# Performance work log

Measured on AMD Instinct MI355X. Metric: run time of the kernel, lower is better.

The kernel has to match this reference:

```python
import jax, jax.numpy as jnp
import numpy as np

DIM = 768
HEADS = 12
TOPK = 32


def setup_inputs() -> dict:
    key = jax.random.key(0)
    k1, k2, k3 = jax.random.split(key, 3)
    B, hw, T = 8, 576, 4
    N = hw + T * hw
    x = jax.random.normal(k1, (B, N, DIM), dtype=jnp.float32)
    qkv_w = jax.random.normal(k2, (3 * DIM, DIM), dtype=jnp.float32) * 0.02
    proj_w = jax.random.normal(k3, (DIM, DIM), dtype=jnp.float32) * 0.02
    proj_b = jnp.zeros((DIM,), dtype=jnp.float32)
    return {"x": x, "qkv_w": qkv_w, "proj_w": proj_w, "proj_b": proj_b, "T": T, "hw": hw}


def _query_topk_every_frame(attn, hw, T):
    # attn: [B, H, hw, hw + T*hw]
    B, H, n1, _ = attn.shape
    qa = attn[..., :hw]                       # [B,H,hw,hw] query self part
    ma = attn[..., hw:].reshape(B, H, n1, T, hw)  # per-frame memory scores
    vals, idx = jax.lax.top_k(ma, TOPK)       # [B,H,hw,T,K]
    cat = jnp.concatenate([qa, vals.reshape(B, H, n1, T * TOPK)], axis=-1)
    sm = jax.nn.softmax(cat, axis=-1)         # softmax over hw + T*K survivors
    qa2 = sm[..., :hw]
    tv = sm[..., hw:].reshape(B, H, n1, T, TOPK)
    # scatter normalized top-k values back into dense per-frame affinity
    bi = jnp.arange(B)[:, None, None, None, None]
    hi = jnp.arange(H)[None, :, None, None, None]
    ni = jnp.arange(n1)[None, None, :, None, None]
    ti = jnp.arange(T)[None, None, None, :, None]
    aff = jnp.zeros_like(ma).at[bi, hi, ni, ti, idx].set(tv)
    return jnp.concatenate([qa2, aff.reshape(B, H, n1, T * hw)], axis=-1)


def reference(x, qkv_w, proj_w, proj_b, T, hw):
    B, N, C = x.shape
    assert N == hw + T * hw
    hd = C // HEADS
    scale = hd ** -0.5
    qkv = (x @ qkv_w.T).reshape(B, N, 3, HEADS, hd).transpose(2, 0, 3, 1, 4)
    q, k, v = qkv[0], qkv[1], qkv[2]          # each [B,H,N,hd]
    query_q = q[:, :, :hw]                    # [B,H,hw,hd]
    attn = jnp.einsum('bhqd,bhkd->bhqk', query_q, k) * scale  # [B,H,hw,N]
    attn = _query_topk_every_frame(attn, hw, T)
    out = jnp.einsum('bhqk,bhkd->bhqd', attn, v)  # [B,H,hw,hd]
    query = out.transpose(0, 2, 1, 3).reshape(B, hw, C)
    query = query @ proj_w.T + proj_b
    # memory tokens pass through unchanged
    return jnp.concatenate([query, x[:, hw:]], axis=1)
```

## Files before the change

kernel.cpp:

```cpp
#include <hip/hip_runtime.h>
#include <hip/hip_bf16.h>


using s16x8 = __attribute__((ext_vector_type(8))) short;
using f32x4 = __attribute__((ext_vector_type(4))) float;
typedef unsigned short u16;

#define MFMA_B16(A,B,C) __builtin_amdgcn_mfma_f32_16x16x32_bf16(A,B,C,0,0,0)

__device__ __forceinline__ u16 f2bf(float f) {
  unsigned u = __float_as_uint(f);
  u += 0x7FFFu + ((u >> 16) & 1u);
  return (u16)(u >> 16);
}
__device__ __forceinline__ float bf2f(u16 h) {
  return __uint_as_float(((unsigned)h) << 16);
}
__device__ __forceinline__ int lanes_below(unsigned long long m) {
  return __builtin_amdgcn_mbcnt_hi((unsigned)(m >> 32),
         __builtin_amdgcn_mbcnt_lo((unsigned)m, 0));
}

__global__ __launch_bounds__(256) void cvt_kernel(const float* __restrict__ src,
                                                  u16* __restrict__ dst, int n4) {
  int i = blockIdx.x * blockDim.x + threadIdx.x;
  if (i >= n4) return;
  float4 v = ((const float4*)src)[i];
  unsigned lo = (unsigned)f2bf(v.x) | ((unsigned)f2bf(v.y) << 16);
  unsigned hi = (unsigned)f2bf(v.z) | ((unsigned)f2bf(v.w) << 16);
  uint2 o; o.x = lo; o.y = hi;
  ((uint2*)dst)[i] = o;
}

__global__ __launch_bounds__(256) void copy_tail_kernel(const float* __restrict__ x,
                                                        float* __restrict__ out) {
  int i = blockIdx.x * blockDim.x + threadIdx.x;
  int b = i / 442368;
  int off = i - b * 442368;
  size_t e = (size_t)b * 552960 + 110592 + off;
  ((float4*)out)[e] = ((const float4*)x)[e];
}

template<int MODE>
__global__ __launch_bounds__(256) void gemm_nt(
    const u16* __restrict__ A, const u16* __restrict__ Bw,
    const float* __restrict__ bias,
    u16* __restrict__ qbuf, u16* __restrict__ kbuf,
    u16* __restrict__ vbuf, u16* __restrict__ vtb,
    float* __restrict__ fout)
{
  constexpr int LDT = 72;
  __shared__ __align__(16) u16 sA[64 * LDT];
  __shared__ __align__(16) u16 sB[64 * LDT];
  const int n0 = blockIdx.x * 64;
  const int m0 = blockIdx.y * 64;
  if (MODE == 0) {
    if (n0 < 768 && (blockIdx.y % 45) >= 9) return;
  }
  const int tid = threadIdx.x;
  const int w = tid >> 6, lane = tid & 63;
  const int srow = tid >> 2, scb = tid & 3;
  const int mh = (w >> 1) * 32, nh = (w & 1) * 32;
  f32x4 z = {0.f, 0.f, 0.f, 0.f};
  f32x4 acc[2][2] = {{z, z}, {z, z}};

  for (int k0 = 0; k0 < 768; k0 += 64) {
    __syncthreads();
    #pragma unroll
    for (int c = scb; c < 8; c += 4) {
      *(int4*)&sA[srow * LDT + c * 8] =
          *(const int4*)&A[(size_t)(m0 + srow) * 768 + k0 + c * 8];
      *(int4*)&sB[srow * LDT + c * 8] =
          *(const int4*)&Bw[(size_t)(n0 + srow) * 768 + k0 + c * 8];
    }
    __syncthreads();
    #pragma unroll
    for (int kk = 0; kk < 2; ++kk) {
      const int ko = kk * 32 + (lane >> 4) * 8;
      s16x8 a0 = *(const s16x8*)&sA[(mh +      (lane & 15)) * LDT + ko];
      s16x8 a1 = *(const s16x8*)&sA[(mh + 16 + (lane & 15)) * LDT + ko];
      s16x8 b0 = *(const s16x8*)&sB[(nh +      (lane & 15)) * LDT + ko];
      s16x8 b1 = *(const s16x8*)&sB[(nh + 16 + (lane & 15)) * LDT + ko];
      acc[0][0] = MFMA_B16(a0, b0, acc[0][0]);
      acc[0][1] = MFMA_B16(a0, b1, acc[0][1]);
      acc[1][0] = MFMA_B16(a1, b0, acc[1][0]);
      acc[1][1] = MFMA_B16(a1, b1, acc[1][1]);
    }
  }

  if (MODE == 0) {
    const int which = n0 / 768;
    const int h = (n0 % 768) >> 6;
    #pragma unroll
    for (int mi = 0; mi < 2; ++mi)
      #pragma unroll
      for (int ni = 0; ni < 2; ++ni)
        #pragma unroll
        for (int r = 0; r < 4; ++r) {
          const int gm = m0 + mh + mi * 16 + (lane >> 4) * 4 + r;
          const int d  = nh + ni * 16 + (lane & 15);
          const int b  = gm / 2880;
          const int rr = gm - b * 2880;
          const float c = acc[mi][ni][r];
          if (which == 0) {
            if (rr < 576)
              qbuf[((size_t)(b * 12 + h) * 576 + rr) * 64 + d] = f2bf(c * 0.125f);
          } else if (which == 1) {
            kbuf[((size_t)(b * 12 + h) * 2880 + rr) * 64 + d] = f2bf(c);
          } else {
            const u16 bv = f2bf(c);
            vbuf[((size_t)(b * 12 + h) * 2880 + rr) * 64 + d] = bv;
            if (rr < 576)
              vtb[((size_t)((b * 12 + h) * 64 + d)) * 576 + rr] = bv;
          }
        }
  } else {
    #pragma unroll
    for (int mi = 0; mi < 2; ++mi)
      #pragma unroll
      for (int ni = 0; ni < 2; ++ni)
        #pragma unroll
        for (int r = 0; r < 4; ++r) {
          const int gm = m0 + mh + mi * 16 + (lane >> 4) * 4 + r;
          const int gn = n0 + nh + ni * 16 + (lane & 15);
          const int b = gm / 576;
          const int q = gm - b * 576;
          fout[((size_t)b * 2880 + q) * 768 + gn] = acc[mi][ni][r] + bias[gn];
        }
  }
}

__global__ __launch_bounds__(256, 6) void attn_kernel(
    const u16* __restrict__ qbuf, const u16* __restrict__ kbuf,
    const u16* __restrict__ vbuf, const u16* __restrict__ vtb,
    u16* __restrict__ aout)
{
  constexpr int PST = 584;
  __shared__ __align__(16) u16 s_p[16 * PST];
  __shared__ float s_selp[16][32];
  __shared__ u16   s_seli[16][32];
  __shared__ float s_O[16][64];
  __shared__ float s_denom[16];

  const int bid = blockIdx.x;
  const int L = (bid & 7) * 432 + (bid >> 3);
  const int qt = L % 36;
  const int h  = (L / 36) % 12;
  const int b  = L / 432;
  const int bh = b * 12 + h;
  const int q0 = qt * 16;
  const int tid = threadIdx.x, w = tid >> 6, lane = tid & 63;
  const int l15 = lane & 15, rg = lane >> 4;
  const int ko = rg * 8;

  #pragma unroll
  for (int i = 0; i < 4; ++i) ((float*)s_O)[tid + 256 * i] = 0.f;

  const u16* qp = qbuf + ((size_t)bh * 576 + q0) * 64;
  s16x8 aQ[2];
  aQ[0] = *(const s16x8*)&qp[l15 * 64 + ko];
  aQ[1] = *(const s16x8*)&qp[l15 * 64 + 32 + ko];

  const u16* kp = kbuf + (size_t)bh * 2880 * 64;
  f32x4 zz = {0.f, 0.f, 0.f, 0.f};
  f32x4 accO = zz;

  for (int c = 0; c < 5; ++c) {
    #pragma unroll 3
    for (int t = 0; t < 9; ++t) {
      const int wk = w * 144 + t * 16;
      const u16* kr = kp + (size_t)(c * 576 + wk + l15) * 64 + ko;
      s16x8 kf0 = *(const s16x8*)&kr[0];
      s16x8 kf1 = *(const s16x8*)&kr[32];
      f32x4 a0 = zz;
      a0 = MFMA_B16(aQ[0], kf0, a0);
      a0 = MFMA_B16(aQ[1], kf1, a0);
      if (c == 0) {
        #pragma unroll
        for (int r = 0; r < 4; ++r)
          s_p[(rg * 4 + r) * PST + wk + l15] = f2bf(__expf(a0[r]));
      } else {
        #pragma unroll
        for (int r = 0; r < 4; ++r)
          s_p[(rg * 4 + r) * PST + wk + l15] = f2bf(a0[r]);
      }
    }
    __syncthreads();

    if (c == 0) {
      const u16* vt = vtb + ((size_t)bh * 64 + w * 16 + l15) * 576;
      #pragma unroll 3
      for (int k0 = 0; k0 < 576; k0 += 32) {
        s16x8 vf = *(const s16x8*)&vt[k0 + ko];
        s16x8 pa = *(const s16x8*)&s_p[l15 * PST + k0 + ko];
        accO = MFMA_B16(pa, vf, accO);
      }
      #pragma unroll
      for (int ri = 0; ri < 4; ++ri) {
        const int q = w * 4 + ri;
        float s = 0.f;
        #pragma unroll
        for (int j = 0; j < 9; ++j) s += bf2f(s_p[q * PST + lane + 64 * j]);
        #pragma unroll
        for (int off = 1; off < 64; off <<= 1) s += __shfl_xor(s, off);
        if (lane == 0) s_denom[q] = s;
      }
    } else {
      for (int ri = 0; ri < 4; ++ri) {
        const int q = w * 4 + ri;
        unsigned key[9];
        #pragma unroll
        for (int j = 0; j < 9; ++j) {
          unsigned raw = s_p[q * PST + lane + 64 * j];
          key[j] = (raw & 0x8000u) ? (raw ^ 0xFFFFu) : (raw | 0x8000u);
        }
        unsigned prefix = 0;
        for (int bit = 15; bit >= 0; --bit) {
          const unsigned cand = prefix | (1u << bit);
          int cnt = 0;
          #pragma unroll
          for (int j = 0; j < 9; ++j)
            cnt += __popcll(__ballot(key[j] >= cand));
          if (cnt >= 32) prefix = cand;
          if (cnt == 32) break;
        }
        unsigned long long gtm[9], eqm[9];
        int cnt_gt = 0;
        #pragma unroll
        for (int j = 0; j < 9; ++j) {
          gtm[j] = __ballot(key[j] > prefix);
          eqm[j] = __ballot(key[j] == prefix);
          cnt_gt += __popcll(gtm[j]);
        }
        int run_gt = 0, run_eq = cnt_gt;
        float dsum = 0.f;
        #pragma unroll
        for (int j = 0; j < 9; ++j) {
          int slot = -1;
          if (key[j] > prefix) slot = run_gt + lanes_below(gtm[j]);
          else if (key[j] == prefix) {
            const int s2 = run_eq + lanes_below(eqm[j]);
            if (s2 < 32) slot = s2;
          }
          if (slot >= 0) {
            const unsigned kk = key[j];
            const u16 raw = (kk & 0x8000u) ? (u16)(kk ^ 0x8000u) : (u16)(kk ^ 0xFFFFu);
            const float p = __expf(bf2f(raw));
            dsum += p;
            s_selp[q][slot] = p;
            s_seli[q][slot] = (u16)(c * 576 + lane + 64 * j);
          }
          run_gt += __popcll(gtm[j]);
          run_eq += __popcll(eqm[j]);
        }
        #pragma unroll
        for (int off = 1; off < 64; off <<= 1) dsum += __shfl_xor(dsum, off);
        if (lane == 0) s_denom[q] += dsum;
        float ga = 0.f;
        const u16* vp = vbuf + (size_t)bh * 2880 * 64 + lane;
        #pragma unroll 8
        for (int i = 0; i < 32; ++i) {
          const float p = s_selp[q][i];
          const int keyi = s_seli[q][i];
          ga += p * bf2f(vp[(size_t)keyi * 64]);
        }
        s_O[q][lane] += ga;
      }
    }
    __syncthreads();
  }

  const int d = w * 16 + l15;
  #pragma unroll
  for (int r = 0; r < 4; ++r) {
    const int row = rg * 4 + r;
    const float val = (accO[r] + s_O[row][d]) / s_denom[row];
    aout[((size_t)(b * 576 + q0 + row)) * 768 + h * 64 + d] = f2bf(val);
  }
}

extern "C" void kernel_launch(void* const* d_in, const int* in_sizes, int n_in,
                              void* d_out, int out_size, void* d_ws, size_t ws_size,
                              hipStream_t stream)
{
  const float* x      = (const float*)d_in[0];
  const float* qkv_w  = (const float*)d_in[1];
  const float* proj_w = (const float*)d_in[2];
  const float* proj_b = (const float*)d_in[3];
  float* out = (float*)d_out;

  char* ws = (char*)d_ws;
  size_t off = 0;
  auto alloc = [&](size_t bytes) -> void* {
    void* p = ws + off;
    off += (bytes + 255) & ~(size_t)255;
    return p;
  };
  u16* xb   = (u16*)alloc((size_t)23040 * 768 * 2);
  u16* wqb  = (u16*)alloc((size_t)2304 * 768 * 2);
  u16* wpb  = (u16*)alloc((size_t)768 * 768 * 2);
  u16* qbuf = (u16*)alloc((size_t)96 * 576 * 64 * 2);
  u16* vtb  = (u16*)alloc((size_t)96 * 64 * 576 * 2);
  u16* aout = (u16*)alloc((size_t)4608 * 768 * 2);
  u16* kbuf = (u16*)d_out;
  u16* vbuf = kbuf + (size_t)96 * 2880 * 64;

  cvt_kernel<<<17280, 256, 0, stream>>>(x, xb, 17694720 / 4);
  cvt_kernel<<<1728, 256, 0, stream>>>(qkv_w, wqb, 1769472 / 4);
  cvt_kernel<<<576, 256, 0, stream>>>(proj_w, wpb, 589824 / 4);
  gemm_nt<0><<<dim3(36, 360), 256, 0, stream>>>(xb, wqb, nullptr,
                                                qbuf, kbuf, vbuf, vtb, nullptr);
  attn_kernel<<<3456, 256, 0, stream>>>(qbuf, kbuf, vbuf, vtb, aout);
  gemm_nt<1><<<dim3(12, 72), 256, 0, stream>>>(aout, wpb, proj_b,
                                               nullptr, nullptr, nullptr, nullptr, out);
  copy_tail_kernel<<<13824, 256, 0, stream>>>(x, out);
}
```

Before: 552.8 us.

## Replace sparse top-k gather with dense masked P·V MFMA per memory frame

After: 533.8 us. 1.04x faster.

```diff
diff --git a/kernel.cpp b/kernel.cpp
--- a/kernel.cpp
+++ b/kernel.cpp
@@ -110,8 +110,7 @@
           } else {
             const u16 bv = f2bf(c);
             vbuf[((size_t)(b * 12 + h) * 2880 + rr) * 64 + d] = bv;
-            if (rr < 576)
-              vtb[((size_t)((b * 12 + h) * 64 + d)) * 576 + rr] = bv;
+            vtb[((size_t)((b * 12 + h) * 64 + d)) * 2880 + rr] = bv;
           }
         }
   } else {
@@ -130,16 +129,13 @@
   }
 }
 
-__global__ __launch_bounds__(256, 6) void attn_kernel(
+__global__ __launch_bounds__(256, 8) void attn_kernel(
     const u16* __restrict__ qbuf, const u16* __restrict__ kbuf,
     const u16* __restrict__ vbuf, const u16* __restrict__ vtb,
     u16* __restrict__ aout)
 {
   constexpr int PST = 584;
   __shared__ __align__(16) u16 s_p[16 * PST];
-  __shared__ float s_selp[16][32];
-  __shared__ u16   s_seli[16][32];
-  __shared__ float s_O[16][64];
   __shared__ float s_denom[16];
 
   const int bid = blockIdx.x;
@@ -153,15 +149,13 @@
   const int l15 = lane & 15, rg = lane >> 4;
   const int ko = rg * 8;
 
-  #pragma unroll
-  for (int i = 0; i < 4; ++i) ((float*)s_O)[tid + 256 * i] = 0.f;
-
   const u16* qp = qbuf + ((size_t)bh * 576 + q0) * 64;
   s16x8 aQ[2];
   aQ[0] = *(const s16x8*)&qp[l15 * 64 + ko];
   aQ[1] = *(const s16x8*)&qp[l15 * 64 + 32 + ko];
 
   const u16* kp = kbuf + (size_t)bh * 2880 * 64;
+  const u16* vt = vtb + ((size_t)bh * 64 + w * 16 + l15) * 2880;
   f32x4 zz = {0.f, 0.f, 0.f, 0.f};
   f32x4 accO = zz;
 
@@ -188,13 +182,6 @@
     __syncthreads();
 
     if (c == 0) {
-      const u16* vt = vtb + ((size_t)bh * 64 + w * 16 + l15) * 576;
-      #pragma unroll 3
-      for (int k0 = 0; k0 < 576; k0 += 32) {
-        s16x8 vf = *(const s16x8*)&vt[k0 + ko];
-        s16x8 pa = *(const s16x8*)&s_p[l15 * PST + k0 + ko];
-        accO = MFMA_B16(pa, vf, accO);
-      }
       #pragma unroll
       for (int ri = 0; ri < 4; ++ri) {
         const int q = w * 4 + ri;
@@ -224,48 +211,40 @@
           if (cnt >= 32) prefix = cand;
           if (cnt == 32) break;
         }
-        unsigned long long gtm[9], eqm[9];
+        unsigned long long eqm[9];
         int cnt_gt = 0;
         #pragma unroll
         for (int j = 0; j < 9; ++j) {
-          gtm[j] = __ballot(key[j] > prefix);
+          cnt_gt += __popcll(__ballot(key[j] > prefix));
           eqm[j] = __ballot(key[j] == prefix);
-          cnt_gt += __popcll(gtm[j]);
-        }
-        int run_gt = 0, run_eq = cnt_gt;
+        }
+        const int rem = 32 - cnt_gt;
+        int run_eq = 0;
         float dsum = 0.f;
         #pragma unroll
         for (int j = 0; j < 9; ++j) {
-          int slot = -1;
-          if (key[j] > prefix) slot = run_gt + lanes_below(gtm[j]);
-          else if (key[j] == prefix) {
-            const int s2 = run_eq + lanes_below(eqm[j]);
-            if (s2 < 32) slot = s2;
-          }
-          if (slot >= 0) {
-            const unsigned kk = key[j];
-            const u16 raw = (kk & 0x8000u) ? (u16)(kk ^ 0x8000u) : (u16)(kk ^ 0xFFFFu);
-            const float p = __expf(bf2f(raw));
-            dsum += p;
-            s_selp[q][slot] = p;
-            s_seli[q][slot] = (u16)(c * 576 + lane + 64 * j);
-          }
-          run_gt += __popcll(gtm[j]);
+          const unsigned kk = key[j];
+          const bool sel = (kk > prefix) ||
+              (kk == prefix && run_eq + lanes_below(eqm[j]) < rem);
+          const u16 raw = (kk & 0x8000u) ? (u16)(kk ^ 0x8000u) : (u16)(kk ^ 0xFFFFu);
+          const float e = __expf(bf2f(raw));
+          const float p = sel ? e : 0.f;
+          dsum += p;
+          s_p[q * PST + lane + 64 * j] = f2bf(p);
           run_eq += __popcll(eqm[j]);
         }
         #pragma unroll
         for (int off = 1; off < 64; off <<= 1) dsum += __shfl_xor(dsum, off);
         if (lane == 0) s_denom[q] += dsum;
-        float ga = 0.f;
-        const u16* vp = vbuf + (size_t)bh * 2880 * 64 + lane;
-        #pragma unroll 8
-        for (int i = 0; i < 32; ++i) {
-          const float p = s_selp[q][i];
-          const int keyi = s_seli[q][i];
-          ga += p * bf2f(vp[(size_t)keyi * 64]);
-        }
-        s_O[q][lane] += ga;
       }
+      __syncthreads();
+    }
+
+    #pragma unroll 3
+    for (int k0 = 0; k0 < 576; k0 += 32) {
+      s16x8 vf = *(const s16x8*)&vt[c * 576 + k0 + ko];
+      s16x8 pa = *(const s16x8*)&s_p[l15 * PST + k0 + ko];
+      accO = MFMA_B16(pa, vf, accO);
     }
     __syncthreads();
   }
@@ -274,7 +253,7 @@
   #pragma unroll
   for (int r = 0; r < 4; ++r) {
     const int row = rg * 4 + r;
-    const float val = (accO[r] + s_O[row][d]) / s_denom[row];
+    const float val = accO[r] / s_denom[row];
     aout[((size_t)(b * 576 + q0 + row)) * 768 + h * 64 + d] = f2bf(val);
   }
 }
@@ -300,7 +279,7 @@
   u16* wqb  = (u16*)alloc((size_t)2304 * 768 * 2);
   u16* wpb  = (u16*)alloc((size_t)768 * 768 * 2);
   u16* qbuf = (u16*)alloc((size_t)96 * 576 * 64 * 2);
-  u16* vtb  = (u16*)alloc((size_t)96 * 64 * 576 * 2);
+  u16* vtb  = (u16*)alloc((size_t)96 * 64 * 2880 * 2);
   u16* aout = (u16*)alloc((size_t)4608 * 768 * 2);
   u16* kbuf = (u16*)d_out;
   u16* vbuf = kbuf + (size_t)96 * 2880 * 64;
```
